# Kernel optimization log

Measured on AMD Instinct MI355X. Metric: run time of the kernel, lower is better.

## Reference

```python
import jax, jax.numpy as jnp
import numpy as np
from math import sqrt

N_HEADS = 16

def setup_inputs() -> dict:
    key = jax.random.key(0)
    ks = jax.random.split(key, 6)
    B, T, C = 4, 2048, 1024
    s = 0.02
    return {
        "X": jax.random.normal(ks[0], (B, T, C), jnp.float32),
        "Wq": jax.random.normal(ks[1], (C, C), jnp.float32) * s,
        "Wk": jax.random.normal(ks[2], (C, C), jnp.float32) * s,
        "Wv": jax.random.normal(ks[3], (C, C), jnp.float32) * s,
        "Wo": jax.random.normal(ks[4], (C, C), jnp.float32) * s,
        "bo": jnp.zeros((C,), jnp.float32),
    }

def reference(X, Wq, Wk, Wv, Wo, bo):
    B, T, C = X.shape
    H = N_HEADS
    D = C // H
    scale = sqrt(C / H)  # == sqrt(D)
    # Linear layers (torch Linear: y = x @ W.T), split into heads: [B,H,T,D]
    Q = (X @ Wq.T).reshape(B, T, H, D).transpose(0, 2, 1, 3)
    K = (X @ Wk.T).reshape(B, T, H, D).transpose(0, 2, 1, 3)
    V = (X @ Wv.T).reshape(B, T, H, D).transpose(0, 2, 1, 3)
    A = jnp.einsum("bhtd,bhsd->bhts", Q, K) / scale  # [B,H,T,T]
    causal = jnp.tril(jnp.ones((T, T), dtype=bool))
    A = jnp.where(causal, A, -jnp.inf)
    A = jax.nn.softmax(A, axis=-1)
    Y = jnp.einsum("bhts,bhsd->bhtd", A, V)  # [B,H,T,D]
    Y = Y.transpose(0, 2, 1, 3).reshape(B, T, C)
    return Y @ Wo.T + bo
```

## Files before the change

### kernel.cpp

```cpp
#include <hip/hip_runtime.h>
#include <hip/hip_bf16.h>
#include <stdint.h>


typedef unsigned short u16;
typedef __attribute__((ext_vector_type(8))) __bf16 bf16x8;
typedef __attribute__((ext_vector_type(4))) float  f32x4;
typedef __attribute__((ext_vector_type(4))) unsigned short u16x4;
typedef __attribute__((ext_vector_type(8))) unsigned short u16x8;
typedef __attribute__((ext_vector_type(4))) short s16x4;

#define B_  4
#define T_  2048
#define C_  1024
#define H_  16
#define D_  64
#define BT_ (B_ * T_)
#define NT_ 16

#define Q_SCALE 0.1803368801111204f

__device__ __forceinline__ u16 f32_to_bf16(float f) {
    unsigned int u = __float_as_uint(f);
    unsigned int r = (u + 0x7FFFu + ((u >> 16) & 1u)) >> 16;
    return (u16)r;
}

__device__ __forceinline__ unsigned int pk_bf16(float a, float b) {
    float2 f2; f2.x = a; f2.y = b;
    __hip_bfloat162 h = __float22bfloat162_rn(f2);
    return *(unsigned int*)&h;
}

__device__ __forceinline__ void async16(const void* g, void* lds) {
    __builtin_amdgcn_global_load_lds(
        (const __attribute__((address_space(1))) void*)g,
        (__attribute__((address_space(3))) void*)lds, 16, 0, 0);
}

__global__ void cast_all_kernel(const float* __restrict__ X,
                                const float* __restrict__ w0, const float* __restrict__ w1,
                                const float* __restrict__ w2, const float* __restrict__ w3,
                                u16* __restrict__ xo,
                                u16* __restrict__ o0, u16* __restrict__ o1,
                                u16* __restrict__ o2, u16* __restrict__ o3) {
    int id = blockIdx.x;
    const float* in; u16* out; int i;
    if (id < 8192) {
        in = X; out = xo; i = id * 256 + threadIdx.x;
    } else {
        int k = (id - 8192) >> 10;
        in  = (k == 0) ? w0 : (k == 1) ? w1 : (k == 2) ? w2 : w3;
        out = (k == 0) ? o0 : (k == 1) ? o1 : (k == 2) ? o2 : o3;
        i = ((id - 8192) & 1023) * 256 + threadIdx.x;
    }
    float4 v = ((const float4*)in)[i];
    u16x4 o;
    o[0] = f32_to_bf16(v.x); o[1] = f32_to_bf16(v.y);
    o[2] = f32_to_bf16(v.z); o[3] = f32_to_bf16(v.w);
    ((u16x4*)out)[i] = o;
}

#define QPHASE(CB, MH, NH, DOISSUE, G, GATE)                                      \
  {                                                                               \
    if ((NH) == 0) {                                                              \
      _Pragma("unroll")                                                           \
      for (int f = 0; f < 4; ++f) {                                               \
        _Pragma("unroll")                                                         \
        for (int ks = 0; ks < 2; ++ks)                                            \
          xf[f][ks] = *(const bf16x8*)((CB) + (MH) * 16384 + axoff[f][ks]);       \
      }                                                                           \
    }                                                                             \
    if ((MH) == 0) {                                                              \
      _Pragma("unroll")                                                           \
      for (int e = 0; e < 2; ++e) {                                               \
        _Pragma("unroll")                                                         \
        for (int ks = 0; ks < 2; ++ks)                                            \
          wf[NH][e][ks] = *(const bf16x8*)((CB) + (NH) * 16384 + bwoff[e][ks]);   \
      }                                                                           \
    }                                                                             \
    if (DOISSUE) issue_unit(G);                                                   \
    if ((GATE) == 4)      asm volatile("s_waitcnt vmcnt(4)" ::: "memory");        \
    else if ((GATE) == 2) asm volatile("s_waitcnt vmcnt(2)" ::: "memory");        \
    else if ((GATE) == 0) asm volatile("s_waitcnt vmcnt(0)" ::: "memory");        \
    __builtin_amdgcn_s_barrier();                                                 \
    asm volatile("" ::: "memory");                                                \
    __builtin_amdgcn_s_setprio(1);                                                \
    _Pragma("unroll")                                                             \
    for (int f = 0; f < 4; ++f) {                                                 \
      _Pragma("unroll")                                                           \
      for (int e = 0; e < 2; ++e) {                                               \
        f32x4 a_ = acc[(MH) * 4 + f][(NH) * 2 + e];                               \
        if (SWAPV) {                                                              \
          a_ = __builtin_amdgcn_mfma_f32_16x16x32_bf16(xf[f][0], wf[NH][e][0], a_, 0, 0, 0); \
          a_ = __builtin_amdgcn_mfma_f32_16x16x32_bf16(xf[f][1], wf[NH][e][1], a_, 0, 0, 0); \
        } else {                                                                  \
          a_ = __builtin_amdgcn_mfma_f32_16x16x32_bf16(wf[NH][e][0], xf[f][0], a_, 0, 0, 0); \
          a_ = __builtin_amdgcn_mfma_f32_16x16x32_bf16(wf[NH][e][1], xf[f][1], a_, 0, 0, 0); \
        }                                                                         \
        acc[(MH) * 4 + f][(NH) * 2 + e] = a_;                                     \
      }                                                                           \
    }                                                                             \
    __builtin_amdgcn_s_setprio(0);                                                \
    asm volatile("" ::: "memory");                                                \
    __builtin_amdgcn_s_barrier();                                                 \
    asm volatile("" ::: "memory");                                                \
  }

template<bool SWAPV>
__device__ __forceinline__ void qkv256_core(const u16* __restrict__ Arow,
                                            const u16* __restrict__ Brow,
                                            char* lds, f32x4 (&acc)[8][4])
{
    int tid  = threadIdx.x;
    int lane = tid & 63, w = tid >> 6;
    int quad = lane >> 4, l15 = lane & 15;
    int wm = w >> 2, wn = w & 3;

    int gc = (((tid & 7) - (tid >> 3)) & 7) * 8;
    const u16* xsrc0 = Arow + (size_t)(tid >> 3) * C_ + gc;
    const u16* xsrc1 = xsrc0 + (size_t)64 * C_;
    const u16* wsrc0 = Brow + (size_t)(tid >> 3) * C_ + gc;
    const u16* wsrc1 = wsrc0 + (size_t)64 * C_;

    auto issue_unit = [&](int g) {
        int u = g & 3, kt = g >> 2;
        char* d = lds + ((kt & 1) << 16) + (u << 14) + (w << 10);
        size_t off = (size_t)(u & 1) * (128 * C_) + (size_t)kt * 64;
        const u16* s0 = (u < 2) ? xsrc0 : wsrc0;
        const u16* s1 = (u < 2) ? xsrc1 : wsrc1;
        async16(s0 + off, d);
        async16(s1 + off, d + 8192);
    };

    int axoff[4][2], bwoff[2][2];
#pragma unroll
    for (int f = 0; f < 4; ++f) {
        int r = wm * 64 + f * 16 + l15;
#pragma unroll
        for (int ks = 0; ks < 2; ++ks)
            axoff[f][ks] = r * 128 + (((ks * 4 + quad + r) & 7) << 4);
    }
#pragma unroll
    for (int e = 0; e < 2; ++e) {
        int r = wn * 32 + e * 16 + l15;
#pragma unroll
        for (int ks = 0; ks < 2; ++ks)
            bwoff[e][ks] = 32768 + r * 128 + (((ks * 4 + quad + r) & 7) << 4);
    }

    bf16x8 xf[4][2];
    bf16x8 wf[2][2][2];

    issue_unit(0); issue_unit(2); issue_unit(3); issue_unit(1);
    asm volatile("s_waitcnt vmcnt(4)" ::: "memory");
    __builtin_amdgcn_s_barrier();
    asm volatile("" ::: "memory");

    for (int t = 0; t < NT_ - 1; ++t) {
        char* cb = lds + ((t & 1) << 16);
        int g4 = (t + 1) << 2;
        QPHASE(cb, 0, 0, 1, g4 + 0, 4);
        QPHASE(cb, 0, 1, 1, g4 + 2, 4);
        QPHASE(cb, 1, 0, 1, g4 + 3, -1);
        QPHASE(cb, 1, 1, 1, g4 + 1, 4);
    }
    {
        char* cb = lds + (((NT_ - 1) & 1) << 16);
        QPHASE(cb, 0, 0, 0, 0, 2);
        QPHASE(cb, 0, 1, 0, 0, 0);
        QPHASE(cb, 1, 0, 0, 0, -1);
        QPHASE(cb, 1, 1, 0, 0, -1);
    }
}

__global__ __launch_bounds__(512, 2) void qkv_gemm256(
    const u16* __restrict__ Xb,
    const u16* __restrict__ Wqb, const u16* __restrict__ Wkb, const u16* __restrict__ Wvb,
    u16* __restrict__ Qb, u16* __restrict__ Kb, u16* __restrict__ Vtb)
{
    __shared__ __attribute__((aligned(128))) char LDSRAW[131072];

    int id = blockIdx.x;
    int wg = (id & 7) * 48 + (id >> 3);
    int bm = wg / 12, bn = wg % 12;
    int m0 = bm * 256;
    int nmat = bn >> 2;
    int chb  = (bn & 3) * 256;

    const u16* Wsel = (nmat == 0) ? Wqb : (nmat == 1) ? Wkb : Wvb;
    const u16* Arow = Xb   + (size_t)m0  * C_;
    const u16* Brow = Wsel + (size_t)chb * C_;

    f32x4 acc[8][4];
    const f32x4 z4 = {0.f, 0.f, 0.f, 0.f};
#pragma unroll
    for (int i = 0; i < 8; ++i)
#pragma unroll
        for (int j = 0; j < 4; ++j) acc[i][j] = z4;

    int tid = threadIdx.x, lane = tid & 63, w = tid >> 6;
    int quad = lane >> 4, l15 = lane & 15;
    int wm = w >> 2, wn = w & 3;

    if (nmat < 2) {
        qkv256_core<false>(Arow, Brow, LDSRAW, acc);
        u16* OUT = nmat ? Kb : Qb;
        float scale = nmat ? 1.0f : Q_SCALE;
#pragma unroll
        for (int mi = 0; mi < 8; ++mi) {
            size_t trow = (size_t)(m0 + (mi >> 2) * 128 + wm * 64 + (mi & 3) * 16 + l15) * C_;
#pragma unroll
            for (int nj = 0; nj < 4; ++nj) {
                int ch = chb + (nj >> 1) * 128 + wn * 32 + (nj & 1) * 16 + quad * 4;
                u16x4 v;
#pragma unroll
                for (int rr = 0; rr < 4; ++rr) v[rr] = f32_to_bf16(acc[mi][nj][rr] * scale);
                *(u16x4*)&OUT[trow + ch] = v;
            }
        }
    } else {
        qkv256_core<true>(Arow, Brow, LDSRAW, acc);
#pragma unroll
        for (int mi = 0; mi < 8; ++mi) {
            int t0 = m0 + (mi >> 2) * 128 + wm * 64 + (mi & 3) * 16 + quad * 4;
            int bb_ = t0 >> 11, tloc = t0 & (T_ - 1);
#pragma unroll
            for (int nj = 0; nj < 4; ++nj) {
                int ch = chb + (nj >> 1) * 128 + wn * 32 + (nj & 1) * 16 + l15;
                int h = ch >> 6, d = ch & 63;
                u16x4 v;
#pragma unroll
                for (int rr = 0; rr < 4; ++rr) v[rr] = f32_to_bf16(acc[mi][nj][rr]);
                *(u16x4*)&Vtb[(size_t)((bb_ * H_ + h) * D_ + d) * T_ + tloc] = v;
            }
        }
    }
}

template<bool SWAP>
__device__ __forceinline__ void gemm8_core(const u16* __restrict__ Arow,
                                           const u16* __restrict__ Brow,
                                           char* lds, f32x4 (&acc)[4][4])
{
    int tid  = threadIdx.x;
    int lane = tid & 63, w = tid >> 6;
    int quad = lane >> 4, l15 = lane & 15;
    int wm = w >> 2, wn = w & 3;

    int r  = tid >> 2, s4 = tid & 3;
    int kg = ((s4 - (r >> 1)) & 3) * 8;
    const u16* xsrc  = Arow + (size_t)r * C_ + kg;
    const u16* wsrc0 = Brow + (size_t)r * C_ + kg;
    const u16* wsrc1 = Brow + (size_t)(128 + r) * C_ + kg;
    int wu = w << 10;

    int xoff[4], woff[4];
#pragma unroll
    for (int i = 0; i < 4; ++i) {
        int rx = wm * 64 + i * 16 + l15;
        xoff[i] = rx * 64 + (((rx >> 1) + quad) & 3) * 16;
        int rw = wn * 64 + i * 16 + l15;
        woff[i] = 16384 + rw * 64 + (((rw >> 1) + quad) & 3) * 16;
    }

    auto issue_group = [&](int g) {
        int db = (g >> 1) & 1, ks = g & 1;
        int koff = (g >> 1) * 64 + ks * 32;
        char* ldb = lds + db * 49152;
        async16(xsrc  + koff, ldb + ks * 8192 + wu);
        async16(wsrc0 + koff, ldb + 16384 + ks * 16384 + wu);
        async16(wsrc1 + koff, ldb + 16384 + ks * 16384 + 8192 + wu);
    };

    issue_group(0); issue_group(1); issue_group(2);
    asm volatile("s_waitcnt vmcnt(6)" ::: "memory");
    __builtin_amdgcn_s_barrier();
    asm volatile("" ::: "memory");

    for (int t = 0; t < NT_; ++t) {
        char* cb = lds + (t & 1) * 49152;
#pragma unroll
        for (int p = 0; p < 2; ++p) {
            bf16x8 xf[4], wf[4];
            const char* xb = cb + p * 8192;
            const char* wb = cb + p * 16384;
#pragma unroll
            for (int i = 0; i < 4; ++i) xf[i] = *(const bf16x8*)(xb + xoff[i]);
#pragma unroll
            for (int j = 0; j < 4; ++j) wf[j] = *(const bf16x8*)(wb + woff[j]);

            int g = 2 * t + 3 + p;
            if (g < 2 * NT_) issue_group(g);

            if (t < NT_ - 2) {
                asm volatile("s_waitcnt vmcnt(6)" ::: "memory");
            } else if (t == NT_ - 2) {
                if (p == 0) asm volatile("s_waitcnt vmcnt(6)" ::: "memory");
                else        asm volatile("s_waitcnt vmcnt(3)" ::: "memory");
            } else {
                if (p == 0) asm volatile("s_waitcnt vmcnt(0)" ::: "memory");
            }
            asm volatile("" ::: "memory");
            __builtin_amdgcn_s_barrier();
            asm volatile("" ::: "memory");

            __builtin_amdgcn_s_setprio(1);
#pragma unroll
            for (int i = 0; i < 4; ++i)
#pragma unroll
                for (int j = 0; j < 4; ++j) {
                    if (SWAP)
                        acc[i][j] = __builtin_amdgcn_mfma_f32_16x16x32_bf16(xf[i], wf[j], acc[i][j], 0, 0, 0);
                    else
                        acc[i][j] = __builtin_amdgcn_mfma_f32_16x16x32_bf16(wf[j], xf[i], acc[i][j], 0, 0, 0);
                }
            __builtin_amdgcn_s_setprio(0);
            asm volatile("" ::: "memory");
            __builtin_amdgcn_s_barrier();
            asm volatile("" ::: "memory");
        }
    }
}

__global__ __launch_bounds__(256, 4) void attn_kernel(
    const u16* __restrict__ Qb, const u16* __restrict__ Kb,
    const u16* __restrict__ Vtb, u16* __restrict__ Yb)
{
    __shared__ u16 SMA[16384];
    u16* Ks0 = SMA;
    u16* Ks1 = SMA + 4096;
    u16* Vs0 = SMA + 8192;
    u16* Vs1 = SMA + 12288;

    int id = blockIdx.x;
    int bh = id & 63;
    int jj = id >> 6;

    int tid = threadIdx.x, lane = tid & 63, w = tid >> 6;
    int quad = lane >> 4, l15 = lane & 15;
    int b = bh >> 4, h = bh & 15;

    int koff0[4], koff1[4], voff[4][4];
#pragma unroll
    for (int sblk = 0; sblk < 4; ++sblk) {
        int sr = sblk * 16 + l15;
        koff0[sblk] = (sr * 64 + ((quad + sr) & 7) * 8) * 2;
        koff1[sblk] = (sr * 64 + ((4 + quad + sr) & 7) * 8) * 2;
    }
#pragma unroll
    for (int n = 0; n < 4; ++n)
#pragma unroll
        for (int sblk = 0; sblk < 4; ++sblk) {
            int dr = n * 16 + l15;
            voff[n][sblk] = (dr * 64 + ((sblk * 2 + (quad >> 1) + dr) & 7) * 8 + (quad & 1) * 4) * 2;
        }

    int cA = tid, cB = tid + 256;
    int sA = cA >> 3, sB = cB >> 3;
    int offA = (((cA & 7) - sA) & 7) * 8;
    int offB = (((cB & 7) - sB) & 7) * 8;
    const u16* Kbase = Kb + (size_t)(b * T_) * C_ + h * 64;
    const u16* Vbase = Vtb + (size_t)bh * D_ * T_;
    int ldsb0 = (w * 64) * 16, ldsb1 = (256 + w * 64) * 16;

    const s16x4 ones = { (short)0x3F80, (short)0x3F80, (short)0x3F80, (short)0x3F80 };
    const f32x4 z4 = {0.f, 0.f, 0.f, 0.f};

    int qts[2] = { jj, 31 - jj };

    for (int pass = 0; pass < 2; ++pass) {
        int qt = qts[pass];
        int qbase = qt * 64;

        if (pass) __syncthreads();

        bf16x8 qf0, qf1;
        {
            const u16* q0 = Qb + ((size_t)(b * T_ + qbase + w * 16 + l15)) * C_ + h * 64;
            qf0 = *(const bf16x8*)(q0 + quad * 8);
            qf1 = *(const bf16x8*)(q0 + 32 + quad * 8);
        }

        f32x4 o_acc[4];
        f32x4 l_acc = z4;
#pragma unroll
        for (int n = 0; n < 4; ++n) o_acc[n] = z4;

        const int nst = qt + 1;

        const u16* kgpA = Kbase + (size_t)sA * C_ + offA;
        const u16* kgpB = Kbase + (size_t)sB * C_ + offB;
        const u16* vgpA = Vbase + sA * T_ + offA;
        const u16* vgpB = Vbase + sB * T_ + offB;

        async16(kgpA, (char*)Ks0 + ldsb0);
        async16(kgpB, (char*)Ks0 + ldsb1);
        async16(vgpA, (char*)Vs0 + ldsb0);
        async16(vgpB, (char*)Vs0 + ldsb1);
        kgpA += 64 * C_; kgpB += 64 * C_; vgpA += 64; vgpB += 64;

        auto tile_body = [&](int st, const u16* K_, const u16* V_, char* Kpf, char* Vpf) {
            __syncthreads();
            if (st + 1 < nst) {
                async16(kgpA, Kpf + ldsb0);
                async16(kgpB, Kpf + ldsb1);
                async16(vgpA, Vpf + ldsb0);
                async16(vgpB, Vpf + ldsb1);
            }
            kgpA += 64 * C_; kgpB += 64 * C_; vgpA += 64; vgpB += 64;

            f32x4 sv[4];
#pragma unroll
            for (int sblk = 0; sblk < 4; ++sblk) {
                bf16x8 k0 = *(const bf16x8*)((const char*)K_ + koff0[sblk]);
                bf16x8 k1 = *(const bf16x8*)((const char*)K_ + koff1[sblk]);
                f32x4 t0 = __builtin_amdgcn_mfma_f32_16x16x32_bf16(k0, qf0, z4, 0, 0, 0);
                sv[sblk] = __builtin_amdgcn_mfma_f32_16x16x32_bf16(k1, qf1, t0, 0, 0, 0);
            }

            if (st == qt) {
                int tl = w * 16 + l15;
#pragma unroll
                for (int sblk = 0; sblk < 4; ++sblk)
#pragma unroll
                    for (int r = 0; r < 4; ++r)
                        if (sblk * 16 + quad * 4 + r > tl) sv[sblk][r] = -1e30f;
            }

            s16x4 pfrag[4];
#pragma unroll
            for (int sblk = 0; sblk < 4; ++sblk) {
#pragma unroll
                for (int r = 0; r < 4; ++r)
                    sv[sblk][r] = __builtin_amdgcn_exp2f(sv[sblk][r]);
                uint2 pk;
                pk.x = pk_bf16(sv[sblk][0], sv[sblk][1]);
                pk.y = pk_bf16(sv[sblk][2], sv[sblk][3]);
                pfrag[sblk] = *(s16x4*)&pk;
                l_acc = __builtin_amdgcn_mfma_f32_16x16x16bf16_1k(ones, pfrag[sblk], l_acc, 0, 0, 0);
            }

#pragma unroll
            for (int n = 0; n < 4; ++n)
#pragma unroll
                for (int sblk = 0; sblk < 4; ++sblk) {
                    s16x4 va = *(const s16x4*)((const char*)V_ + voff[n][sblk]);
                    o_acc[n] = __builtin_amdgcn_mfma_f32_16x16x16bf16_1k(va, pfrag[sblk], o_acc[n], 0, 0, 0);
                }
        };

        for (int st = 0; st < nst; st += 2) {
            tile_body(st, Ks0, Vs0, (char*)Ks1, (char*)Vs1);
            if (st + 1 < nst)
                tile_body(st + 1, Ks1, Vs1, (char*)Ks0, (char*)Vs0);
        }

        __syncthreads();
        u16* PW = SMA + w * 1152;
        {
            float inv = 1.0f / l_acc[0];
#pragma unroll
            for (int n = 0; n < 4; ++n) {
                uint2 pk;
                pk.x = pk_bf16(o_acc[n][0] * inv, o_acc[n][1] * inv);
                pk.y = pk_bf16(o_acc[n][2] * inv, o_acc[n][3] * inv);
                *(u16x4*)&PW[l15 * 72 + n * 16 + quad * 4] = *(u16x4*)&pk;
            }
        }
        asm volatile("s_waitcnt lgkmcnt(0)" ::: "memory");
#pragma unroll
        for (int st = 0; st < 2; ++st) {
            int tr = st * 8 + (lane >> 3);
            int d8 = (lane & 7) * 8;
            u16x8 v = *(u16x8*)&PW[tr * 72 + d8];
            *(u16x8*)&Yb[(size_t)(b * T_ + qbase + w * 16 + tr) * C_ + h * 64 + d8] = v;
        }
    }
}

__global__ __launch_bounds__(512, 2) void proj_gemm8(
    const u16* __restrict__ Yb, const u16* __restrict__ Wob,
    const float* __restrict__ bo, float* __restrict__ out)
{
    __shared__ __attribute__((aligned(128))) char LDSRAW[98304];

    int id = blockIdx.x;
    int wg = (id & 7) * 32 + (id >> 3);
    int bm = wg >> 2, bn = wg & 3;
    int m0 = bm * 128, n0 = bn * 256;

    f32x4 acc[4][4];
    const f32x4 z4 = {0.f, 0.f, 0.f, 0.f};
#pragma unroll
    for (int i = 0; i < 4; ++i)
#pragma unroll
        for (int j = 0; j < 4; ++j) acc[i][j] = z4;

    gemm8_core<false>(Yb + (size_t)m0 * C_, Wob + (size_t)n0 * C_, LDSRAW, acc);

    int tid = threadIdx.x, lane = tid & 63, w = tid >> 6;
    int quad = lane >> 4, l15 = lane & 15;
    int wm = w >> 2, wn = w & 3;

#pragma unroll
    for (int j = 0; j < 4; ++j) {
        int ch = n0 + wn * 64 + j * 16 + quad * 4;
        f32x4 bv = *(const f32x4*)&bo[ch];
#pragma unroll
        for (int i = 0; i < 4; ++i) {
            int t = m0 + wm * 64 + i * 16 + l15;
            f32x4 v = acc[i][j] + bv;
            *(f32x4*)&out[(size_t)t * C_ + ch] = v;
        }
    }
}

extern "C" void kernel_launch(void* const* d_in, const int* in_sizes, int n_in,
                              void* d_out, int out_size, void* d_ws, size_t ws_size,
                              hipStream_t stream) {
    const float* X  = (const float*)d_in[0];
    const float* Wq = (const float*)d_in[1];
    const float* Wk = (const float*)d_in[2];
    const float* Wv = (const float*)d_in[3];
    const float* Wo = (const float*)d_in[4];
    const float* bo = (const float*)d_in[5];

    char* ws = (char*)d_ws;
    u16* Xb  = (u16*)(ws);
    u16* Wqb = (u16*)(ws + (16u << 20));
    u16* Wkb = (u16*)(ws + (18u << 20));
    u16* Wvb = (u16*)(ws + (20u << 20));
    u16* Wob = (u16*)(ws + (22u << 20));
    u16* Qb  = (u16*)(ws + (24u << 20));
    u16* Kb  = (u16*)(ws + (40u << 20));
    u16* Vtb = (u16*)(ws + (56u << 20));
    u16* Yb  = (u16*)(ws + (72u << 20));

    cast_all_kernel<<<dim3(8192 + 4 * 1024), 256, 0, stream>>>(
        X, Wq, Wk, Wv, Wo, Xb, Wqb, Wkb, Wvb, Wob);

    qkv_gemm256<<<dim3(384), 512, 0, stream>>>(Xb, Wqb, Wkb, Wvb, Qb, Kb, Vtb);
    attn_kernel<<<dim3(1024), 256, 0, stream>>>(Qb, Kb, Vtb, Yb);
    proj_gemm8<<<dim3(256), 512, 0, stream>>>(Yb, Wob, bo, (float*)d_out);
}
```

Baseline: 241.2 us.

## Split QKV GEMM into Q/K 256-tiles and V 128-row tiles; prefetch LDS fragments in proj GEMM

Measured after the change: 230.4 us, median of 2. 4.5% less time.

```diff
diff --git a/kernel.cpp b/kernel.cpp
--- a/kernel.cpp
+++ b/kernel.cpp
@@ -91,13 +91,8 @@
       _Pragma("unroll")                                                           \
       for (int e = 0; e < 2; ++e) {                                               \
         f32x4 a_ = acc[(MH) * 4 + f][(NH) * 2 + e];                               \
-        if (SWAPV) {                                                              \
-          a_ = __builtin_amdgcn_mfma_f32_16x16x32_bf16(xf[f][0], wf[NH][e][0], a_, 0, 0, 0); \
-          a_ = __builtin_amdgcn_mfma_f32_16x16x32_bf16(xf[f][1], wf[NH][e][1], a_, 0, 0, 0); \
-        } else {                                                                  \
-          a_ = __builtin_amdgcn_mfma_f32_16x16x32_bf16(wf[NH][e][0], xf[f][0], a_, 0, 0, 0); \
-          a_ = __builtin_amdgcn_mfma_f32_16x16x32_bf16(wf[NH][e][1], xf[f][1], a_, 0, 0, 0); \
-        }                                                                         \
+        a_ = __builtin_amdgcn_mfma_f32_16x16x32_bf16(wf[NH][e][0], xf[f][0], a_, 0, 0, 0); \
+        a_ = __builtin_amdgcn_mfma_f32_16x16x32_bf16(wf[NH][e][1], xf[f][1], a_, 0, 0, 0); \
         acc[(MH) * 4 + f][(NH) * 2 + e] = a_;                                     \
       }                                                                           \
     }                                                                             \
@@ -107,13 +102,11 @@
     asm volatile("" ::: "memory");                                                \
   }
 
-template<bool SWAPV>
 __device__ __forceinline__ void qkv256_core(const u16* __restrict__ Arow,
                                             const u16* __restrict__ Brow,
                                             char* lds, f32x4 (&acc)[8][4])
 {
-    int tid  = threadIdx.x;
-    int lane = tid & 63, w = tid >> 6;
+    int tid = threadIdx.x, lane = tid & 63, w = tid >> 6;
     int quad = lane >> 4, l15 = lane & 15;
     int wm = w >> 2, wn = w & 3;
 
@@ -166,7 +159,7 @@
         QPHASE(cb, 1, 1, 1, g4 + 1, 4);
     }
     {
-        char* cb = lds + (((NT_ - 1) & 1) << 16);
+        char* cb = lds + 65536;
         QPHASE(cb, 0, 0, 0, 0, 2);
         QPHASE(cb, 0, 1, 0, 0, 0);
         QPHASE(cb, 1, 0, 0, 0, -1);
@@ -174,74 +167,204 @@
     }
 }
 
-__global__ __launch_bounds__(512, 2) void qkv_gemm256(
-    const u16* __restrict__ Xb,
-    const u16* __restrict__ Wqb, const u16* __restrict__ Wkb, const u16* __restrict__ Wvb,
+__device__ __forceinline__ void qkv128v_core(const u16* __restrict__ Arow,
+                                             const u16* __restrict__ Brow,
+                                             char* lds, f32x4 (&acc)[4][4])
+{
+    int tid = threadIdx.x, lane = tid & 63, w = tid >> 6;
+    int quad = lane >> 4, l15 = lane & 15;
+    int wm = w >> 2, wn = w & 3;
+
+    int gc = (((tid & 7) - (tid >> 3)) & 7) * 8;
+    const u16* asrc  = Arow + (size_t)(tid >> 3) * C_ + gc;
+    const u16* bsrc0 = Brow + (size_t)(tid >> 3) * C_ + gc;
+    const u16* bsrc1 = bsrc0 + (size_t)64 * C_;
+
+    auto issue3 = [&](int kt) {
+        char* db = lds + ((kt & 1) << 16) + (w << 10);
+        int ko = kt * 64;
+        async16(asrc + ko,                       db);
+        async16(asrc + ko + (size_t)64 * C_,     db + 8192);
+        async16(bsrc0 + ko,                      db + 32768);
+        async16(bsrc1 + ko,                      db + 32768 + 8192);
+        async16(bsrc0 + ko + (size_t)128 * C_,   db + 49152);
+        async16(bsrc1 + ko + (size_t)128 * C_,   db + 49152 + 8192);
+    };
+
+    int axoff[4][2], bwoff[2][2];
+#pragma unroll
+    for (int f = 0; f < 4; ++f) {
+        int r = wm * 64 + f * 16 + l15;
+#pragma unroll
+        for (int ks = 0; ks < 2; ++ks)
+            axoff[f][ks] = r * 128 + (((ks * 4 + quad + r) & 7) << 4);
+    }
+#pragma unroll
+    for (int e = 0; e < 2; ++e) {
+        int r = wn * 32 + e * 16 + l15;
+#pragma unroll
+        for (int ks = 0; ks < 2; ++ks)
+            bwoff[e][ks] = 32768 + r * 128 + (((ks * 4 + quad + r) & 7) << 4);
+    }
+
+    bf16x8 xf[4][2], wf[2][2];
+
+    issue3(0);
+
+    for (int t = 0; t < NT_; ++t) {
+        char* cb = lds + ((t & 1) << 16);
+        if (t + 1 < NT_) issue3(t + 1);
+        if (t == NT_ - 1) asm volatile("s_waitcnt vmcnt(0)" ::: "memory");
+        else              asm volatile("s_waitcnt vmcnt(6)" ::: "memory");
+        __builtin_amdgcn_s_barrier();
+        asm volatile("" ::: "memory");
+
+#pragma unroll
+        for (int f = 0; f < 4; ++f)
+#pragma unroll
+            for (int ks = 0; ks < 2; ++ks)
+                xf[f][ks] = *(const bf16x8*)(cb + axoff[f][ks]);
+#pragma unroll
+        for (int e = 0; e < 2; ++e)
+#pragma unroll
+            for (int ks = 0; ks < 2; ++ks)
+                wf[e][ks] = *(const bf16x8*)(cb + bwoff[e][ks]);
+        __builtin_amdgcn_s_setprio(1);
+#pragma unroll
+        for (int f = 0; f < 4; ++f)
+#pragma unroll
+            for (int e = 0; e < 2; ++e) {
+                f32x4 a_ = acc[f][e];
+                a_ = __builtin_amdgcn_mfma_f32_16x16x32_bf16(xf[f][0], wf[e][0], a_, 0, 0, 0);
+                a_ = __builtin_amdgcn_mfma_f32_16x16x32_bf16(xf[f][1], wf[e][1], a_, 0, 0, 0);
+                acc[f][e] = a_;
+            }
+        __builtin_amdgcn_s_setprio(0);
+
+#pragma unroll
+        for (int e = 0; e < 2; ++e)
+#pragma unroll
+            for (int ks = 0; ks < 2; ++ks)
+                wf[e][ks] = *(const bf16x8*)(cb + 16384 + bwoff[e][ks]);
+        __builtin_amdgcn_s_setprio(1);
+#pragma unroll
+        for (int f = 0; f < 4; ++f)
+#pragma unroll
+            for (int e = 0; e < 2; ++e) {
+                f32x4 a_ = acc[f][2 + e];
+                a_ = __builtin_amdgcn_mfma_f32_16x16x32_bf16(xf[f][0], wf[e][0], a_, 0, 0, 0);
+                a_ = __builtin_amdgcn_mfma_f32_16x16x32_bf16(xf[f][1], wf[e][1], a_, 0, 0, 0);
+                acc[f][2 + e] = a_;
+            }
+        __builtin_amdgcn_s_setprio(0);
+        asm volatile("" ::: "memory");
+        __builtin_amdgcn_s_barrier();
+        asm volatile("" ::: "memory");
+    }
+}
+
+__global__ __launch_bounds__(512, 2) void qkv_mix512(
+    const u16* __restrict__ Xb, const u16* __restrict__ Wcat,
     u16* __restrict__ Qb, u16* __restrict__ Kb, u16* __restrict__ Vtb)
 {
     __shared__ __attribute__((aligned(128))) char LDSRAW[131072];
 
     int id = blockIdx.x;
-    int wg = (id & 7) * 48 + (id >> 3);
-    int bm = wg / 12, bn = wg % 12;
-    int m0 = bm * 256;
-    int nmat = bn >> 2;
-    int chb  = (bn & 3) * 256;
-
-    const u16* Wsel = (nmat == 0) ? Wqb : (nmat == 1) ? Wkb : Wvb;
-    const u16* Arow = Xb   + (size_t)m0  * C_;
-    const u16* Brow = Wsel + (size_t)chb * C_;
-
-    f32x4 acc[8][4];
-    const f32x4 z4 = {0.f, 0.f, 0.f, 0.f};
-#pragma unroll
-    for (int i = 0; i < 8; ++i)
-#pragma unroll
-        for (int j = 0; j < 4; ++j) acc[i][j] = z4;
-
     int tid = threadIdx.x, lane = tid & 63, w = tid >> 6;
     int quad = lane >> 4, l15 = lane & 15;
     int wm = w >> 2, wn = w & 3;
 
-    if (nmat < 2) {
-        qkv256_core<false>(Arow, Brow, LDSRAW, acc);
-        u16* OUT = nmat ? Kb : Qb;
-        float scale = nmat ? 1.0f : Q_SCALE;
+    if (id < 256) {
+        int ti = (id & 7) * 32 + (id >> 3);
+        int bm = ti & 31, bn = ti >> 5;
+        int m0 = bm * 256, chb = bn * 256;
+
+        f32x4 acc[8][4];
+        const f32x4 z4 = {0.f, 0.f, 0.f, 0.f};
+#pragma unroll
+        for (int i = 0; i < 8; ++i)
+#pragma unroll
+            for (int j = 0; j < 4; ++j) acc[i][j] = z4;
+
+        qkv256_core(Xb + (size_t)m0 * C_, Wcat + (size_t)chb * C_, LDSRAW, acc);
+
 #pragma unroll
         for (int mi = 0; mi < 8; ++mi) {
             size_t trow = (size_t)(m0 + (mi >> 2) * 128 + wm * 64 + (mi & 3) * 16 + l15) * C_;
 #pragma unroll
             for (int nj = 0; nj < 4; ++nj) {
-                int ch = chb + (nj >> 1) * 128 + wn * 32 + (nj & 1) * 16 + quad * 4;
+                int colb = chb + (nj >> 1) * 128 + wn * 32 + (nj & 1) * 16 + quad * 4;
+                u16* OUT = (colb < 1024) ? Qb : Kb;
+                float sc = (colb < 1024) ? Q_SCALE : 1.0f;
                 u16x4 v;
 #pragma unroll
-                for (int rr = 0; rr < 4; ++rr) v[rr] = f32_to_bf16(acc[mi][nj][rr] * scale);
-                *(u16x4*)&OUT[trow + ch] = v;
+                for (int rr = 0; rr < 4; ++rr) v[rr] = f32_to_bf16(acc[mi][nj][rr] * sc);
+                *(u16x4*)&OUT[trow + (colb & 1023)] = v;
             }
         }
     } else {
-        qkv256_core<true>(Arow, Brow, LDSRAW, acc);
-#pragma unroll
-        for (int mi = 0; mi < 8; ++mi) {
-            int t0 = m0 + (mi >> 2) * 128 + wm * 64 + (mi & 3) * 16 + quad * 4;
-            int bb_ = t0 >> 11, tloc = t0 & (T_ - 1);
+        int id2 = id - 256;
+        int hw = (id2 & 7) * 32 + (id2 >> 3);
+        int vt = hw >> 6;
+        int bm = (hw & 63) >> 1, half = hw & 1;
+        int m0h = bm * 256 + half * 128;
+        int chb = 2048 + vt * 256;
+
+        f32x4 acc[4][4];
+        const f32x4 z4 = {0.f, 0.f, 0.f, 0.f};
+#pragma unroll
+        for (int i = 0; i < 4; ++i)
+#pragma unroll
+            for (int j = 0; j < 4; ++j) acc[i][j] = z4;
+
+        qkv128v_core(Xb + (size_t)m0h * C_, Wcat + (size_t)chb * C_, LDSRAW, acc);
+
+#pragma unroll
+        for (int mi = 0; mi < 4; ++mi) {
+            int t0 = m0h + wm * 64 + mi * 16 + quad * 4;
+            int b_ = t0 >> 11, tl = t0 & (T_ - 1);
 #pragma unroll
             for (int nj = 0; nj < 4; ++nj) {
                 int ch = chb + (nj >> 1) * 128 + wn * 32 + (nj & 1) * 16 + l15;
-                int h = ch >> 6, d = ch & 63;
+                int h = (ch >> 6) & 15, d = ch & 63;
                 u16x4 v;
 #pragma unroll
                 for (int rr = 0; rr < 4; ++rr) v[rr] = f32_to_bf16(acc[mi][nj][rr]);
-                *(u16x4*)&Vtb[(size_t)((bb_ * H_ + h) * D_ + d) * T_ + tloc] = v;
-            }
-        }
-    }
-}
-
-template<bool SWAP>
-__device__ __forceinline__ void gemm8_core(const u16* __restrict__ Arow,
-                                           const u16* __restrict__ Brow,
-                                           char* lds, f32x4 (&acc)[4][4])
+                *(u16x4*)&Vtb[((size_t)(b_ * H_ + h) * D_ + d) * T_ + tl] = v;
+            }
+        }
+    }
+}
+
+#define RD8(CB, KS, FX, FW)                                                      \
+    _Pragma("unroll") for (int i_ = 0; i_ < 4; ++i_) {                           \
+        FX[i_] = *(const bf16x8*)((CB) + (KS) * 8192  + xoff[i_]);               \
+        FW[i_] = *(const bf16x8*)((CB) + (KS) * 16384 + woff[i_]);               \
+    }
+
+#define PPH(ISSUE, GATE, FX, FW, ...)                                            \
+  {                                                                              \
+    ISSUE;                                                                       \
+    if ((GATE) == 6)      asm volatile("s_waitcnt vmcnt(6)" ::: "memory");       \
+    else if ((GATE) == 3) asm volatile("s_waitcnt vmcnt(3)" ::: "memory");       \
+    else if ((GATE) == 0) asm volatile("s_waitcnt vmcnt(0)" ::: "memory");       \
+    __builtin_amdgcn_s_barrier();                                                \
+    asm volatile("" ::: "memory");                                               \
+    __VA_ARGS__;                                                                 \
+    __builtin_amdgcn_sched_barrier(0);                                           \
+    __builtin_amdgcn_s_setprio(1);                                               \
+    _Pragma("unroll") for (int i = 0; i < 4; ++i)                                \
+      _Pragma("unroll") for (int j = 0; j < 4; ++j)                              \
+        acc[i][j] = __builtin_amdgcn_mfma_f32_16x16x32_bf16(FW[j], FX[i], acc[i][j], 0, 0, 0); \
+    __builtin_amdgcn_s_setprio(0);                                               \
+    asm volatile("" ::: "memory");                                               \
+    __builtin_amdgcn_s_barrier();                                                \
+    asm volatile("" ::: "memory");                                               \
+  }
+
+__device__ __forceinline__ void gemm8p_core(const u16* __restrict__ Arow,
+                                            const u16* __restrict__ Brow,
+                                            char* lds, f32x4 (&acc)[4][4])
 {
     int tid  = threadIdx.x;
     int lane = tid & 63, w = tid >> 6;
@@ -273,53 +396,28 @@
         async16(wsrc1 + koff, ldb + 16384 + ks * 16384 + 8192 + wu);
     };
 
+    bf16x8 fAx[4], fAw[4], fBx[4], fBw[4];
+
     issue_group(0); issue_group(1); issue_group(2);
     asm volatile("s_waitcnt vmcnt(6)" ::: "memory");
     __builtin_amdgcn_s_barrier();
     asm volatile("" ::: "memory");
-
-    for (int t = 0; t < NT_; ++t) {
-        char* cb = lds + (t & 1) * 49152;
-#pragma unroll
-        for (int p = 0; p < 2; ++p) {
-            bf16x8 xf[4], wf[4];
-            const char* xb = cb + p * 8192;
-            const char* wb = cb + p * 16384;
-#pragma unroll
-            for (int i = 0; i < 4; ++i) xf[i] = *(const bf16x8*)(xb + xoff[i]);
-#pragma unroll
-            for (int j = 0; j < 4; ++j) wf[j] = *(const bf16x8*)(wb + woff[j]);
-
-            int g = 2 * t + 3 + p;
-            if (g < 2 * NT_) issue_group(g);
-
-            if (t < NT_ - 2) {
-                asm volatile("s_waitcnt vmcnt(6)" ::: "memory");
-            } else if (t == NT_ - 2) {
-                if (p == 0) asm volatile("s_waitcnt vmcnt(6)" ::: "memory");
-                else        asm volatile("s_waitcnt vmcnt(3)" ::: "memory");
-            } else {
-                if (p == 0) asm volatile("s_waitcnt vmcnt(0)" ::: "memory");
-            }
-            asm volatile("" ::: "memory");
-            __builtin_amdgcn_s_barrier();
-            asm volatile("" ::: "memory");
-
-            __builtin_amdgcn_s_setprio(1);
-#pragma unroll
-            for (int i = 0; i < 4; ++i)
-#pragma unroll
-                for (int j = 0; j < 4; ++j) {
-                    if (SWAP)
-                        acc[i][j] = __builtin_amdgcn_mfma_f32_16x16x32_bf16(xf[i], wf[j], acc[i][j], 0, 0, 0);
-                    else
-                        acc[i][j] = __builtin_amdgcn_mfma_f32_16x16x32_bf16(wf[j], xf[i], acc[i][j], 0, 0, 0);
-                }
-            __builtin_amdgcn_s_setprio(0);
-            asm volatile("" ::: "memory");
-            __builtin_amdgcn_s_barrier();
-            asm volatile("" ::: "memory");
-        }
+    RD8(lds, 0, fAx, fAw);
+
+    for (int t = 0; t < NT_ - 1; ++t) {
+        char* cb  = lds + (t & 1) * 49152;
+        char* cbn = lds + ((t + 1) & 1) * 49152;
+        PPH({ issue_group(2 * t + 3); }, 6, fAx, fAw, { RD8(cb, 1, fBx, fBw); });
+        if (t < NT_ - 2) {
+            PPH({ issue_group(2 * t + 4); }, 6, fBx, fBw, { RD8(cbn, 0, fAx, fAw); });
+        } else {
+            PPH({}, 3, fBx, fBw, { RD8(cbn, 0, fAx, fAw); });
+        }
+    }
+    {
+        char* cb = lds + ((NT_ - 1) & 1) * 49152;
+        PPH({}, 0, fAx, fAw, { RD8(cb, 1, fBx, fBw); });
+        PPH({}, -1, fBx, fBw, {});
     }
 }
 
@@ -497,7 +595,7 @@
 #pragma unroll
         for (int j = 0; j < 4; ++j) acc[i][j] = z4;
 
-    gemm8_core<false>(Yb + (size_t)m0 * C_, Wob + (size_t)n0 * C_, LDSRAW, acc);
+    gemm8p_core(Yb + (size_t)m0 * C_, Wob + (size_t)n0 * C_, LDSRAW, acc);
 
     int tid = threadIdx.x, lane = tid & 63, w = tid >> 6;
     int quad = lane >> 4, l15 = lane & 15;
@@ -540,7 +638,7 @@
     cast_all_kernel<<<dim3(8192 + 4 * 1024), 256, 0, stream>>>(
         X, Wq, Wk, Wv, Wo, Xb, Wqb, Wkb, Wvb, Wob);
 
-    qkv_gemm256<<<dim3(384), 512, 0, stream>>>(Xb, Wqb, Wkb, Wvb, Qb, Kb, Vtb);
+    qkv_mix512<<<dim3(512), 512, 0, stream>>>(Xb, Wqb, Qb, Kb, Vtb);
     attn_kernel<<<dim3(1024), 256, 0, stream>>>(Qb, Kb, Vtb, Yb);
     proj_gemm8<<<dim3(256), 512, 0, stream>>>(Yb, Wob, bo, (float*)d_out);
 }
```
